# Optimization experiments

Measured on AMD Instinct MI355X. Metric: run time of the kernel, lower is better.

Reference implementation:

```python
import jax, jax.numpy as jnp
import numpy as np

BITS = 4
SIGNED_MIN, SIGNED_MAX = -(2 ** (BITS - 1)), 2 ** (BITS - 1) - 1      # int4: [-8, 7]
UNSIGNED_MIN, UNSIGNED_MAX = 0, 2 ** BITS - 1                          # uint4: [0, 15]
INT32_MIN, INT32_MAX = -(2.0 ** 31), 2.0 ** 31 - 1


def fake_quant(x, scale, qmin, qmax):
    """Brevitas-style fake quantization with straight-through rounding."""
    q = jnp.clip(jnp.round(x / scale), qmin, qmax) * scale
    # STE: identity gradient through round/clip
    return x + jax.lax.stop_gradient(q - x)


def weight_scale(W):
    # Brevitas default weight quantizer: per-tensor scale from max-abs stats
    return jax.lax.stop_gradient(jnp.max(jnp.abs(W))) / SIGNED_MAX


def setup_inputs() -> dict:
    key = jax.random.key(0)
    ks = jax.random.split(key, 5)
    B, S, D, F = 4, 2048, 2048, 8192
    return {
        "x": jax.random.normal(ks[0], (B, S, D), dtype=jnp.float32),
        "W1": jax.random.normal(ks[1], (F, D), dtype=jnp.float32) * 0.02,
        "b1": jax.random.normal(ks[2], (F,), dtype=jnp.float32) * 0.02,
        "W2": jax.random.normal(ks[3], (D, F), dtype=jnp.float32) * 0.02,
        "b2": jax.random.normal(ks[4], (D,), dtype=jnp.float32) * 0.02,
        "s_act1": jnp.full((1,), 0.1, dtype=jnp.float32),
        "s_act2": jnp.full((1,), 0.1, dtype=jnp.float32),
    }


def reference(x, W1, b1, W2, b2, s_act1, s_act2):
    s1 = s_act1[0]
    s2 = s_act2[0]

    # quantizer_1: signed int4 QuantIdentity on input
    x_q = fake_quant(x, s1, SIGNED_MIN, SIGNED_MAX)

    # w_1: int4 weight QuantLinear with Int32Bias (bias scale = in_scale * w_scale)
    sw1 = weight_scale(W1)
    W1_q = fake_quant(W1, sw1, SIGNED_MIN, SIGNED_MAX)
    b1_q = fake_quant(b1, s1 * sw1, INT32_MIN, INT32_MAX)
    h = jnp.einsum("bsd,fd->bsf", x_q, W1_q) + b1_q  # [B, S, d_ff]

    # quantizer_2: QuantReLU -> unsigned int4 fake-quant of relu(h)
    h_q = fake_quant(jax.nn.relu(h), s2, UNSIGNED_MIN, UNSIGNED_MAX)
    # dropout: identity in eval mode

    # w_2: int4 weight QuantLinear, input scale = s2
    sw2 = weight_scale(W2)
    W2_q = fake_quant(W2, sw2, SIGNED_MIN, SIGNED_MAX)
    b2_q = fake_quant(b2, s2 * sw2, INT32_MIN, INT32_MAX)
    out = jnp.einsum("bsf,df->bsd", h_q, W2_q) + b2_q  # [B, S, d_model]
    return out
```

## Files before the change

kernel.cpp:

```cpp
#include <hip/hip_runtime.h>

typedef int int32x4 __attribute__((ext_vector_type(4)));

__global__ void maxabs_kernel(const float* __restrict__ x, int n4,
                              unsigned* __restrict__ out) {
    float m = 0.f;
    int i = blockIdx.x * blockDim.x + threadIdx.x;
    int stride = gridDim.x * blockDim.x;
    const float4* x4 = (const float4*)x;
    for (int j = i; j < n4; j += stride) {
        float4 v = x4[j];
        m = fmaxf(m, fmaxf(fmaxf(fabsf(v.x), fabsf(v.y)),
                           fmaxf(fabsf(v.z), fabsf(v.w))));
    }
#pragma unroll
    for (int off = 32; off; off >>= 1)
        m = fmaxf(m, __shfl_down(m, off, 64));
    __shared__ float wm[4];
    int ln = threadIdx.x & 63, wv = threadIdx.x >> 6;
    if (ln == 0) wm[wv] = m;
    __syncthreads();
    if (threadIdx.x == 0) {
        float bm = fmaxf(fmaxf(wm[0], wm[1]), fmaxf(wm[2], wm[3]));
        atomicMax(out, __float_as_uint(bm));
    }
}

__global__ void quant_kernel(const float* __restrict__ x, int n4,
                             const float* __restrict__ sptr, float sdiv,
                             float lo, float hi, char* __restrict__ out) {
    float s = sptr[0] / sdiv;
    int i = blockIdx.x * blockDim.x + threadIdx.x;
    int stride = gridDim.x * blockDim.x;
    const float4* x4 = (const float4*)x;
    int* o4 = (int*)out;
    for (int j = i; j < n4; j += stride) {
        float4 v = x4[j];
        int a = (int)fminf(fmaxf(rintf(v.x / s), lo), hi);
        int b = (int)fminf(fmaxf(rintf(v.y / s), lo), hi);
        int c = (int)fminf(fmaxf(rintf(v.z / s), lo), hi);
        int d = (int)fminf(fmaxf(rintf(v.w / s), lo), hi);
        o4[j] = (a & 255) | ((b & 255) << 8) | ((c & 255) << 16) | ((d & 255) << 24);
    }
}

template <bool FIRST>
__global__ __launch_bounds__(256, 2)
void gemm_i8_kernel(const char* __restrict__ A, const char* __restrict__ B,
                    int M, int N, int K,
                    const float* __restrict__ sa_ptr,
                    const float* __restrict__ wmax_ptr,
                    const float* __restrict__ bias,
                    const float* __restrict__ s2_ptr,
                    char* __restrict__ out8, float* __restrict__ outf) {
    __shared__ __align__(16) char lA[128 * 128];
    __shared__ __align__(16) char lB[128 * 128];

    const int tid = threadIdx.x;
    const int wv = tid >> 6, ln = tid & 63;
    const int m0 = blockIdx.y * 128;
    const int n0 = blockIdx.x * 128;
    const int wr = wv >> 1, wc = wv & 1;

    int32x4 acc[4][4] = {};

    const int nkt = K >> 7;
    for (int kt = 0; kt < nkt; ++kt) {
        const int k0 = kt << 7;
#pragma unroll
        for (int r = 0; r < 4; ++r) {
            int s = r * 256 + tid;
            int row = s >> 3;
            int ch = s & 7;
            int sch = ch ^ (row & 7);
            long ga = (long)(m0 + row) * K + k0 + sch * 16;
            long gb = (long)(n0 + row) * K + k0 + sch * 16;
            int lbase = (r * 256 + wv * 64) * 16;
            __builtin_amdgcn_global_load_lds(
                (const __attribute__((address_space(1))) void*)(A + ga),
                (__attribute__((address_space(3))) void*)(lA + lbase), 16, 0, 0);
            __builtin_amdgcn_global_load_lds(
                (const __attribute__((address_space(1))) void*)(B + gb),
                (__attribute__((address_space(3))) void*)(lB + lbase), 16, 0, 0);
        }
        __syncthreads();

        int32x4 af[4][2], bf[4][2];
#pragma unroll
        for (int mf = 0; mf < 4; ++mf)
#pragma unroll
            for (int kk = 0; kk < 2; ++kk) {
                int row = wr * 64 + mf * 16 + (ln & 15);
                int ch = kk * 4 + (ln >> 4);
                af[mf][kk] = *(const int32x4*)(lA + row * 128 + ((ch ^ (row & 7)) * 16));
            }
#pragma unroll
        for (int nf = 0; nf < 4; ++nf)
#pragma unroll
            for (int kk = 0; kk < 2; ++kk) {
                int col = wc * 64 + nf * 16 + (ln & 15);
                int ch = kk * 4 + (ln >> 4);
                bf[nf][kk] = *(const int32x4*)(lB + col * 128 + ((ch ^ (col & 7)) * 16));
            }

#pragma unroll
        for (int kk = 0; kk < 2; ++kk)
#pragma unroll
            for (int mf = 0; mf < 4; ++mf)
#pragma unroll
                for (int nf = 0; nf < 4; ++nf)
                    acc[mf][nf] = __builtin_amdgcn_mfma_i32_16x16x64_i8(
                        af[mf][kk], bf[nf][kk], acc[mf][nf], 0, 0, 0);
        __syncthreads();
    }

    float sa = sa_ptr[0];
    float sw = wmax_ptr[0] / 7.0f;
    float sab = sa * sw;
    float s2 = FIRST ? s2_ptr[0] : 0.f;

#pragma unroll
    for (int nf = 0; nf < 4; ++nf) {
        int col = n0 + wc * 64 + nf * 16 + (ln & 15);
        float bq = rintf(bias[col] / sab) * sab;
#pragma unroll
        for (int mf = 0; mf < 4; ++mf) {
            int rbase = m0 + wr * 64 + mf * 16 + ((ln >> 4) << 2);
#pragma unroll
            for (int i = 0; i < 4; ++i) {
                float h = sab * (float)acc[mf][nf][i] + bq;
                long off = (long)(rbase + i) * N + col;
                if constexpr (FIRST) {
                    h = fmaxf(h, 0.f);
                    float q = fminf(fmaxf(rintf(h / s2), 0.f), 15.f);
                    out8[off] = (char)(int)q;
                } else {
                    outf[off] = h;
                }
            }
        }
    }
}

extern "C" void kernel_launch(void* const* d_in, const int* in_sizes, int n_in,
                              void* d_out, int out_size, void* d_ws, size_t ws_size,
                              hipStream_t stream) {
    const float* x  = (const float*)d_in[0];
    const float* W1 = (const float*)d_in[1];
    const float* b1 = (const float*)d_in[2];
    const float* W2 = (const float*)d_in[3];
    const float* b2 = (const float*)d_in[4];
    const float* s1 = (const float*)d_in[5];
    const float* s2 = (const float*)d_in[6];

    const int M = 8192, D = 2048, F = 8192;

    char* ws = (char*)d_ws;
    unsigned* mx1 = (unsigned*)ws;
    unsigned* mx2 = (unsigned*)(ws + 4);
    char* xq  = ws + 256;
    char* w1q = xq + (size_t)M * D;
    char* w2q = w1q + (size_t)F * D;
    char* hq  = w2q + (size_t)D * F;

    hipMemsetAsync(d_ws, 0, 8, stream);

    maxabs_kernel<<<2048, 256, 0, stream>>>(W1, (F * D) >> 2, mx1);
    maxabs_kernel<<<2048, 256, 0, stream>>>(W2, (D * F) >> 2, mx2);

    quant_kernel<<<2048, 256, 0, stream>>>(x,  (M * D) >> 2, s1, 1.f, -8.f, 7.f, xq);
    quant_kernel<<<2048, 256, 0, stream>>>(W1, (F * D) >> 2, (const float*)mx1, 7.f, -8.f, 7.f, w1q);
    quant_kernel<<<2048, 256, 0, stream>>>(W2, (D * F) >> 2, (const float*)mx2, 7.f, -8.f, 7.f, w2q);

    gemm_i8_kernel<true><<<dim3(F / 128, M / 128), 256, 0, stream>>>(
        xq, w1q, M, F, D, s1, (const float*)mx1, b1, s2, hq, nullptr);

    gemm_i8_kernel<false><<<dim3(D / 128, M / 128), 256, 0, stream>>>(
        hq, w2q, M, D, F, s2, (const float*)mx2, b2, nullptr, nullptr, (float*)d_out);
}
```

Baseline: 378.1 us.

## Pipeline int8 GEMM with 4-stage LDS ring buffer and BK=64 prefetch

Restructures the int8 MFMA GEMM main loop into a 4-slot shared-memory ring. Each slot holds a 64-wide K tile, and loads run three tiles ahead using async global-to-LDS copies. Explicit vmcnt waits, barriers and setprio around the MFMA block let global loads overlap with compute instead of serialising behind them. LDS use and per-tile swizzle logic stay about the same, at the cost of more barriers per K step and hand-tuned waitcnt counts.

```diff
diff --git a/kernel.cpp b/kernel.cpp
--- a/kernel.cpp
+++ b/kernel.cpp
@@ -44,6 +44,41 @@
     }
 }
 
+#define GEMM_STEP(T_, VMC_, DO_STAGE_)                                        \
+  {                                                                           \
+    const int t_ = (T_);                                                      \
+    if (DO_STAGE_) stage(t_ + 3);                                             \
+    asm volatile("s_waitcnt vmcnt(" VMC_ ")" ::: "memory");                   \
+    __builtin_amdgcn_s_barrier();                                             \
+    __builtin_amdgcn_sched_barrier(0);                                        \
+    const char* la_ = lA[t_ & 3];                                             \
+    const char* lb_ = lB[t_ & 3];                                             \
+    int32x4 af[4], bf[4];                                                     \
+    _Pragma("unroll")                                                         \
+    for (int mf = 0; mf < 4; ++mf) {                                          \
+      int row = wr * 64 + mf * 16 + lnlo;                                     \
+      int c = lnhi ^ ((row >> 1) & 3);                                        \
+      af[mf] = *(const int32x4*)(la_ + row * 64 + c * 16);                    \
+    }                                                                         \
+    _Pragma("unroll")                                                         \
+    for (int nf = 0; nf < 4; ++nf) {                                          \
+      int col = wc * 64 + nf * 16 + lnlo;                                     \
+      int c = lnhi ^ ((col >> 1) & 3);                                        \
+      bf[nf] = *(const int32x4*)(lb_ + col * 64 + c * 16);                    \
+    }                                                                         \
+    asm volatile("s_waitcnt lgkmcnt(0)" ::: "memory");                        \
+    __builtin_amdgcn_s_barrier();                                             \
+    __builtin_amdgcn_sched_barrier(0);                                        \
+    __builtin_amdgcn_s_setprio(1);                                            \
+    _Pragma("unroll")                                                         \
+    for (int mf = 0; mf < 4; ++mf)                                            \
+      _Pragma("unroll")                                                       \
+      for (int nf = 0; nf < 4; ++nf)                                          \
+        acc[mf][nf] = __builtin_amdgcn_mfma_i32_16x16x64_i8(                  \
+            af[mf], bf[nf], acc[mf][nf], 0, 0, 0);                            \
+    __builtin_amdgcn_s_setprio(0);                                            \
+  }
+
 template <bool FIRST>
 __global__ __launch_bounds__(256, 2)
 void gemm_i8_kernel(const char* __restrict__ A, const char* __restrict__ B,
@@ -53,66 +88,53 @@
                     const float* __restrict__ bias,
                     const float* __restrict__ s2_ptr,
                     char* __restrict__ out8, float* __restrict__ outf) {
-    __shared__ __align__(16) char lA[128 * 128];
-    __shared__ __align__(16) char lB[128 * 128];
+    __shared__ __align__(16) char lA[4][128 * 64];
+    __shared__ __align__(16) char lB[4][128 * 64];
 
     const int tid = threadIdx.x;
     const int wv = tid >> 6, ln = tid & 63;
+    const int lnlo = ln & 15, lnhi = ln >> 4;
     const int m0 = blockIdx.y * 128;
     const int n0 = blockIdx.x * 128;
     const int wr = wv >> 1, wc = wv & 1;
 
     int32x4 acc[4][4] = {};
 
-    const int nkt = K >> 7;
-    for (int kt = 0; kt < nkt; ++kt) {
-        const int k0 = kt << 7;
-#pragma unroll
-        for (int r = 0; r < 4; ++r) {
+    const int nkt = K >> 6;
+
+    auto stage = [&](int t) {
+        const int slot = t & 3;
+        const long k0 = (long)t << 6;
+#pragma unroll
+        for (int r = 0; r < 2; ++r) {
             int s = r * 256 + tid;
-            int row = s >> 3;
-            int ch = s & 7;
-            int sch = ch ^ (row & 7);
-            long ga = (long)(m0 + row) * K + k0 + sch * 16;
-            long gb = (long)(n0 + row) * K + k0 + sch * 16;
+            int row = s >> 2;
+            int cs = s & 3;
+            int c = cs ^ ((row >> 1) & 3);
+            long ga = (long)(m0 + row) * K + k0 + c * 16;
+            long gb = (long)(n0 + row) * K + k0 + c * 16;
             int lbase = (r * 256 + wv * 64) * 16;
             __builtin_amdgcn_global_load_lds(
                 (const __attribute__((address_space(1))) void*)(A + ga),
-                (__attribute__((address_space(3))) void*)(lA + lbase), 16, 0, 0);
+                (__attribute__((address_space(3))) void*)(lA[slot] + lbase), 16, 0, 0);
             __builtin_amdgcn_global_load_lds(
                 (const __attribute__((address_space(1))) void*)(B + gb),
-                (__attribute__((address_space(3))) void*)(lB + lbase), 16, 0, 0);
+                (__attribute__((address_space(3))) void*)(lB[slot] + lbase), 16, 0, 0);
         }
-        __syncthreads();
-
-        int32x4 af[4][2], bf[4][2];
-#pragma unroll
-        for (int mf = 0; mf < 4; ++mf)
-#pragma unroll
-            for (int kk = 0; kk < 2; ++kk) {
-                int row = wr * 64 + mf * 16 + (ln & 15);
-                int ch = kk * 4 + (ln >> 4);
-                af[mf][kk] = *(const int32x4*)(lA + row * 128 + ((ch ^ (row & 7)) * 16));
-            }
-#pragma unroll
-        for (int nf = 0; nf < 4; ++nf)
-#pragma unroll
-            for (int kk = 0; kk < 2; ++kk) {
-                int col = wc * 64 + nf * 16 + (ln & 15);
-                int ch = kk * 4 + (ln >> 4);
-                bf[nf][kk] = *(const int32x4*)(lB + col * 128 + ((ch ^ (col & 7)) * 16));
-            }
-
-#pragma unroll
-        for (int kk = 0; kk < 2; ++kk)
-#pragma unroll
-            for (int mf = 0; mf < 4; ++mf)
-#pragma unroll
-                for (int nf = 0; nf < 4; ++nf)
-                    acc[mf][nf] = __builtin_amdgcn_mfma_i32_16x16x64_i8(
-                        af[mf][kk], bf[nf][kk], acc[mf][nf], 0, 0, 0);
-        __syncthreads();
-    }
+    };
+
+    stage(0);
+    stage(1);
+    stage(2);
+
+    int t = 0;
+    const int nmain = nkt - 3;
+    for (; t < nmain; ++t) {
+        GEMM_STEP(t, "12", true);
+    }
+    GEMM_STEP(t, "8", false); ++t;
+    GEMM_STEP(t, "4", false); ++t;
+    GEMM_STEP(t, "0", false);
 
     float sa = sa_ptr[0];
     float sw = wmax_ptr[0] / 7.0f;
@@ -121,11 +143,11 @@
 
 #pragma unroll
     for (int nf = 0; nf < 4; ++nf) {
-        int col = n0 + wc * 64 + nf * 16 + (ln & 15);
+        int col = n0 + wc * 64 + nf * 16 + lnlo;
         float bq = rintf(bias[col] / sab) * sab;
 #pragma unroll
         for (int mf = 0; mf < 4; ++mf) {
-            int rbase = m0 + wr * 64 + mf * 16 + ((ln >> 4) << 2);
+            int rbase = m0 + wr * 64 + mf * 16 + (lnhi << 2);
 #pragma unroll
             for (int i = 0; i < 4; ++i) {
                 float h = sab * (float)acc[mf][nf][i] + bq;
```

Measured after the change: 492.3 us. 1.3x slower.

## Enlarge int8 GEMM tiles to 256x256 with double-buffered phased LDS pipeline

Applied to the files above, without the earlier changes.

The int8 MFMA GEMMs move from 128x128 tiles with 4 waves and a single LDS buffer to 256x256 tiles with 8 waves. The LDS is double-buffered and split into K halves. Each K step runs as four phases that issue the next tile's async global-to-LDS loads while the current MFMAs execute, using explicit barriers, waitcnts and setprio. The goal is to hide global load latency and raise arithmetic intensity per byte loaded. The cost is higher LDS and register use per block, fewer blocks in the grid, and pipelining that depends on fragile hand-placed waitcnt and barrier ordering.

```diff
diff --git a/kernel.cpp b/kernel.cpp
--- a/kernel.cpp
+++ b/kernel.cpp
@@ -44,8 +44,37 @@
     }
 }
 
+#define PHASE(B_, KH_, MH_, LOADB_, STG_, VMC_)                                \
+  {                                                                            \
+    if (LOADB_) {                                                              \
+      _Pragma("unroll")                                                        \
+      for (int nf = 0; nf < 4; ++nf)                                           \
+        bf[nf] = *(const int32x4*)(&lB[B_][KH_][0] +                           \
+                                   (wn * 64 + nf * 16) * 64 + coff);           \
+    }                                                                          \
+    int32x4 af[4];                                                             \
+    _Pragma("unroll")                                                          \
+    for (int mf = 0; mf < 4; ++mf)                                             \
+      af[mf] = *(const int32x4*)(&lA[B_][KH_][0] +                             \
+                                 (wm * 128 + MH_ * 64 + mf * 16) * 64 + coff); \
+    STG_;                                                                      \
+    __builtin_amdgcn_s_barrier();                                              \
+    asm volatile("s_waitcnt lgkmcnt(0)" ::: "memory");                         \
+    __builtin_amdgcn_sched_barrier(0);                                         \
+    __builtin_amdgcn_s_setprio(1);                                             \
+    _Pragma("unroll")                                                          \
+    for (int mf = 0; mf < 4; ++mf)                                             \
+      _Pragma("unroll")                                                        \
+      for (int nf = 0; nf < 4; ++nf)                                           \
+        acc[MH_ * 4 + mf][nf] = __builtin_amdgcn_mfma_i32_16x16x64_i8(         \
+            af[mf], bf[nf], acc[MH_ * 4 + mf][nf], 0, 0, 0);                   \
+    __builtin_amdgcn_s_setprio(0);                                             \
+    VMC_;                                                                      \
+    __builtin_amdgcn_s_barrier();                                              \
+  }
+
 template <bool FIRST>
-__global__ __launch_bounds__(256, 2)
+__global__ __launch_bounds__(512, 2)
 void gemm_i8_kernel(const char* __restrict__ A, const char* __restrict__ B,
                     int M, int N, int K,
                     const float* __restrict__ sa_ptr,
@@ -53,86 +82,97 @@
                     const float* __restrict__ bias,
                     const float* __restrict__ s2_ptr,
                     char* __restrict__ out8, float* __restrict__ outf) {
-    __shared__ __align__(16) char lA[128 * 128];
-    __shared__ __align__(16) char lB[128 * 128];
+    __shared__ __align__(16) char lA[2][2][256 * 64];
+    __shared__ __align__(16) char lB[2][2][256 * 64];
 
     const int tid = threadIdx.x;
     const int wv = tid >> 6, ln = tid & 63;
-    const int m0 = blockIdx.y * 128;
-    const int n0 = blockIdx.x * 128;
-    const int wr = wv >> 1, wc = wv & 1;
-
-    int32x4 acc[4][4] = {};
+    const int lo = ln & 15, hi = ln >> 4;
+    const int wm = wv >> 2, wn = wv & 3;
+    const long m0 = (long)blockIdx.y * 256;
+    const long n0 = (long)blockIdx.x * 256;
+
+    int32x4 acc[8][4] = {};
+    int32x4 bf[4];
+    const int coff = lo * 64 + ((hi ^ ((lo >> 1) & 3)) << 4);
 
     const int nkt = K >> 7;
-    for (int kt = 0; kt < nkt; ++kt) {
-        const int k0 = kt << 7;
-#pragma unroll
-        for (int r = 0; r < 4; ++r) {
-            int s = r * 256 + tid;
-            int row = s >> 3;
-            int ch = s & 7;
-            int sch = ch ^ (row & 7);
-            long ga = (long)(m0 + row) * K + k0 + sch * 16;
-            long gb = (long)(n0 + row) * K + k0 + sch * 16;
-            int lbase = (r * 256 + wv * 64) * 16;
+
+    auto stg_a = [&](int t, int kh) {
+#pragma unroll
+        for (int r = 0; r < 2; ++r) {
+            int s = r * 512 + tid;
+            int row = s >> 2;
+            int c = (s & 3) ^ ((row >> 1) & 3);
+            long g = (m0 + row) * K + ((long)t << 7) + (kh << 6) + c * 16;
             __builtin_amdgcn_global_load_lds(
-                (const __attribute__((address_space(1))) void*)(A + ga),
-                (__attribute__((address_space(3))) void*)(lA + lbase), 16, 0, 0);
+                (const __attribute__((address_space(1))) void*)(A + g),
+                (__attribute__((address_space(3))) void*)(
+                    &lA[t & 1][kh][0] + (r * 512 + wv * 64) * 16), 16, 0, 0);
+        }
+    };
+    auto stg_b = [&](int t, int kh) {
+#pragma unroll
+        for (int r = 0; r < 2; ++r) {
+            int s = r * 512 + tid;
+            int row = s >> 2;
+            int c = (s & 3) ^ ((row >> 1) & 3);
+            long g = (n0 + row) * K + ((long)t << 7) + (kh << 6) + c * 16;
             __builtin_amdgcn_global_load_lds(
-                (const __attribute__((address_space(1))) void*)(B + gb),
-                (__attribute__((address_space(3))) void*)(lB + lbase), 16, 0, 0);
+                (const __attribute__((address_space(1))) void*)(B + g),
+                (__attribute__((address_space(3))) void*)(
+                    &lB[t & 1][kh][0] + (r * 512 + wv * 64) * 16), 16, 0, 0);
         }
-        __syncthreads();
-
-        int32x4 af[4][2], bf[4][2];
-#pragma unroll
-        for (int mf = 0; mf < 4; ++mf)
-#pragma unroll
-            for (int kk = 0; kk < 2; ++kk) {
-                int row = wr * 64 + mf * 16 + (ln & 15);
-                int ch = kk * 4 + (ln >> 4);
-                af[mf][kk] = *(const int32x4*)(lA + row * 128 + ((ch ^ (row & 7)) * 16));
-            }
-#pragma unroll
-        for (int nf = 0; nf < 4; ++nf)
-#pragma unroll
-            for (int kk = 0; kk < 2; ++kk) {
-                int col = wc * 64 + nf * 16 + (ln & 15);
-                int ch = kk * 4 + (ln >> 4);
-                bf[nf][kk] = *(const int32x4*)(lB + col * 128 + ((ch ^ (col & 7)) * 16));
-            }
-
-#pragma unroll
-        for (int kk = 0; kk < 2; ++kk)
-#pragma unroll
-            for (int mf = 0; mf < 4; ++mf)
-#pragma unroll
-                for (int nf = 0; nf < 4; ++nf)
-                    acc[mf][nf] = __builtin_amdgcn_mfma_i32_16x16x64_i8(
-                        af[mf][kk], bf[nf][kk], acc[mf][nf], 0, 0, 0);
-        __syncthreads();
+    };
+
+    stg_a(0, 0); stg_b(0, 0); stg_a(0, 1); stg_b(0, 1);
+    stg_a(1, 0); stg_b(1, 0);
+    asm volatile("s_waitcnt vmcnt(4)" ::: "memory");
+    __builtin_amdgcn_s_barrier();
+
+    for (int t = 0; t < nkt - 2; ++t) {
+        const int b = t & 1;
+        PHASE(b, 0, 0, true,  stg_a(t + 1, 1), );
+        PHASE(b, 0, 1, false, stg_b(t + 1, 1), );
+        PHASE(b, 1, 0, true,  stg_a(t + 2, 0), );
+        PHASE(b, 1, 1, false, stg_b(t + 2, 0),
+              asm volatile("s_waitcnt vmcnt(4)" ::: "memory"));
+    }
+    {
+        const int t = nkt - 2, b = t & 1;
+        PHASE(b, 0, 0, true,  stg_a(t + 1, 1), );
+        PHASE(b, 0, 1, false, stg_b(t + 1, 1), );
+        PHASE(b, 1, 0, true,  , );
+        PHASE(b, 1, 1, false, ,
+              asm volatile("s_waitcnt vmcnt(0)" ::: "memory"));
+    }
+    {
+        const int b = (nkt - 1) & 1;
+        PHASE(b, 0, 0, true,  , );
+        PHASE(b, 0, 1, false, , );
+        PHASE(b, 1, 0, true,  , );
+        PHASE(b, 1, 1, false, , );
     }
 
     float sa = sa_ptr[0];
     float sw = wmax_ptr[0] / 7.0f;
     float sab = sa * sw;
-    float s2 = FIRST ? s2_ptr[0] : 0.f;
+    float s2v = FIRST ? s2_ptr[0] : 0.f;
 
 #pragma unroll
     for (int nf = 0; nf < 4; ++nf) {
-        int col = n0 + wc * 64 + nf * 16 + (ln & 15);
+        long col = n0 + wn * 64 + nf * 16 + lo;
         float bq = rintf(bias[col] / sab) * sab;
 #pragma unroll
-        for (int mf = 0; mf < 4; ++mf) {
-            int rbase = m0 + wr * 64 + mf * 16 + ((ln >> 4) << 2);
+        for (int am = 0; am < 8; ++am) {
+            long rbase = m0 + wm * 128 + (am >> 2) * 64 + (am & 3) * 16 + (hi << 2);
 #pragma unroll
             for (int i = 0; i < 4; ++i) {
-                float h = sab * (float)acc[mf][nf][i] + bq;
-                long off = (long)(rbase + i) * N + col;
+                float h = sab * (float)acc[am][nf][i] + bq;
+                long off = (rbase + i) * N + col;
                 if constexpr (FIRST) {
                     h = fmaxf(h, 0.f);
-                    float q = fminf(fmaxf(rintf(h / s2), 0.f), 15.f);
+                    float q = fminf(fmaxf(rintf(h / s2v), 0.f), 15.f);
                     out8[off] = (char)(int)q;
                 } else {
                     outf[off] = h;
@@ -172,9 +212,9 @@
     quant_kernel<<<2048, 256, 0, stream>>>(W1, (F * D) >> 2, (const float*)mx1, 7.f, -8.f, 7.f, w1q);
     quant_kernel<<<2048, 256, 0, stream>>>(W2, (D * F) >> 2, (const float*)mx2, 7.f, -8.f, 7.f, w2q);
 
-    gemm_i8_kernel<true><<<dim3(F / 128, M / 128), 256, 0, stream>>>(
+    gemm_i8_kernel<true><<<dim3(F / 256, M / 256), 512, 0, stream>>>(
         xq, w1q, M, F, D, s1, (const float*)mx1, b1, s2, hq, nullptr);
 
-    gemm_i8_kernel<false><<<dim3(D / 128, M / 128), 256, 0, stream>>>(
+    gemm_i8_kernel<false><<<dim3(D / 256, M / 256), 512, 0, stream>>>(
         hq, w2q, M, D, F, s2, (const float*)mx2, b2, nullptr, nullptr, (float*)d_out);
 }
```

Result: slower. 455.5 us (+20.5%).

## Switch GEMM to 32x32x32 int8 MFMA and add XCD-aware workgroup remapping

Applied to the files above, without the earlier changes.

Replaces the 16x16x64 int8 MFMA tiles with 32x32x32 int8 MFMA, so each wave computes its 64x64 sub-tile with 2x2 larger fragments and fewer LDS fragment loads per MFMA. It also remaps workgroup IDs so that consecutive tiles land on the same XCD, aiming for better L2 reuse of A/B rows. The epilogue row/column mapping is rewritten to match the 32x32 accumulator layout, which risks layout errors and gives a different store coalescing pattern.

```diff
diff --git a/kernel.cpp b/kernel.cpp
--- a/kernel.cpp
+++ b/kernel.cpp
@@ -1,6 +1,7 @@
 #include <hip/hip_runtime.h>
 
 typedef int int32x4 __attribute__((ext_vector_type(4)));
+typedef int int32x16 __attribute__((ext_vector_type(16)));
 
 __global__ void maxabs_kernel(const float* __restrict__ x, int n4,
                               unsigned* __restrict__ out) {
@@ -58,23 +59,31 @@
 
     const int tid = threadIdx.x;
     const int wv = tid >> 6, ln = tid & 63;
-    const int m0 = blockIdx.y * 128;
-    const int n0 = blockIdx.x * 128;
+    const int l31 = ln & 31, hi5 = ln >> 5;
     const int wr = wv >> 1, wc = wv & 1;
 
-    int32x4 acc[4][4] = {};
+    const int gx = gridDim.x;
+    const int nwg = gx * gridDim.y;
+    const int orig = blockIdx.y * gx + blockIdx.x;
+    const int q = nwg >> 3, r8 = nwg & 7;
+    const int xcd = orig & 7, idx = orig >> 3;
+    const int wg = (xcd < r8 ? xcd * (q + 1) : r8 * (q + 1) + (xcd - r8) * q) + idx;
+    const long m0 = (long)(wg / gx) * 128;
+    const long n0 = (long)(wg % gx) * 128;
+
+    int32x16 acc[2][2] = {};
 
     const int nkt = K >> 7;
     for (int kt = 0; kt < nkt; ++kt) {
-        const int k0 = kt << 7;
+        const long k0 = (long)kt << 7;
 #pragma unroll
         for (int r = 0; r < 4; ++r) {
             int s = r * 256 + tid;
             int row = s >> 3;
             int ch = s & 7;
             int sch = ch ^ (row & 7);
-            long ga = (long)(m0 + row) * K + k0 + sch * 16;
-            long gb = (long)(n0 + row) * K + k0 + sch * 16;
+            long ga = (m0 + row) * K + k0 + sch * 16;
+            long gb = (n0 + row) * K + k0 + sch * 16;
             int lbase = (r * 256 + wv * 64) * 16;
             __builtin_amdgcn_global_load_lds(
                 (const __attribute__((address_space(1))) void*)(A + ga),
@@ -85,55 +94,56 @@
         }
         __syncthreads();
 
-        int32x4 af[4][2], bf[4][2];
+        int32x4 af[2][4], bf[2][4];
 #pragma unroll
-        for (int mf = 0; mf < 4; ++mf)
+        for (int fm = 0; fm < 2; ++fm)
 #pragma unroll
-            for (int kk = 0; kk < 2; ++kk) {
-                int row = wr * 64 + mf * 16 + (ln & 15);
-                int ch = kk * 4 + (ln >> 4);
-                af[mf][kk] = *(const int32x4*)(lA + row * 128 + ((ch ^ (row & 7)) * 16));
+            for (int ks = 0; ks < 4; ++ks) {
+                int row = wr * 64 + fm * 32 + l31;
+                int ch = ks * 2 + hi5;
+                af[fm][ks] = *(const int32x4*)(lA + row * 128 + ((ch ^ (row & 7)) * 16));
             }
 #pragma unroll
-        for (int nf = 0; nf < 4; ++nf)
+        for (int fn = 0; fn < 2; ++fn)
 #pragma unroll
-            for (int kk = 0; kk < 2; ++kk) {
-                int col = wc * 64 + nf * 16 + (ln & 15);
-                int ch = kk * 4 + (ln >> 4);
-                bf[nf][kk] = *(const int32x4*)(lB + col * 128 + ((ch ^ (col & 7)) * 16));
+            for (int ks = 0; ks < 4; ++ks) {
+                int col = wc * 64 + fn * 32 + l31;
+                int ch = ks * 2 + hi5;
+                bf[fn][ks] = *(const int32x4*)(lB + col * 128 + ((ch ^ (col & 7)) * 16));
             }
 
 #pragma unroll
-        for (int kk = 0; kk < 2; ++kk)
+        for (int ks = 0; ks < 4; ++ks)
 #pragma unroll
-            for (int mf = 0; mf < 4; ++mf)
+            for (int fm = 0; fm < 2; ++fm)
 #pragma unroll
-                for (int nf = 0; nf < 4; ++nf)
-                    acc[mf][nf] = __builtin_amdgcn_mfma_i32_16x16x64_i8(
-                        af[mf][kk], bf[nf][kk], acc[mf][nf], 0, 0, 0);
+                for (int fn = 0; fn < 2; ++fn)
+                    acc[fm][fn] = __builtin_amdgcn_mfma_i32_32x32x32_i8(
+                        af[fm][ks], bf[fn][ks], acc[fm][fn], 0, 0, 0);
         __syncthreads();
     }
 
     float sa = sa_ptr[0];
     float sw = wmax_ptr[0] / 7.0f;
     float sab = sa * sw;
-    float s2 = FIRST ? s2_ptr[0] : 0.f;
+    float s2v = FIRST ? s2_ptr[0] : 0.f;
 
 #pragma unroll
-    for (int nf = 0; nf < 4; ++nf) {
-        int col = n0 + wc * 64 + nf * 16 + (ln & 15);
+    for (int fn = 0; fn < 2; ++fn) {
+        long col = n0 + wc * 64 + fn * 32 + l31;
         float bq = rintf(bias[col] / sab) * sab;
 #pragma unroll
-        for (int mf = 0; mf < 4; ++mf) {
-            int rbase = m0 + wr * 64 + mf * 16 + ((ln >> 4) << 2);
+        for (int fm = 0; fm < 2; ++fm) {
+            long rbase = m0 + wr * 64 + fm * 32 + 4 * hi5;
 #pragma unroll
-            for (int i = 0; i < 4; ++i) {
-                float h = sab * (float)acc[mf][nf][i] + bq;
-                long off = (long)(rbase + i) * N + col;
+            for (int reg = 0; reg < 16; ++reg) {
+                long row = rbase + (reg & 3) + 8 * (reg >> 2);
+                float h = sab * (float)acc[fm][fn][reg] + bq;
+                long off = row * N + col;
                 if constexpr (FIRST) {
                     h = fmaxf(h, 0.f);
-                    float q = fminf(fmaxf(rintf(h / s2), 0.f), 15.f);
-                    out8[off] = (char)(int)q;
+                    float qv = fminf(fmaxf(rintf(h / s2v), 0.f), 15.f);
+                    out8[off] = (char)(int)qv;
                 } else {
                     outf[off] = h;
                 }
```

New measurement: 429.6 us. +13.6%, slower.
